# Performance work log

Hardware: AMD Instinct MI355X
Metric: run time of the kernel (lower is better)

Reference implementation:

```python
import jax, jax.numpy as jnp
import numpy as np

K = 20  # number of nearest neighbors (includes self, distance 0, as in torch topk(largest=False))


def edge_feature(x, k):
    """x: (B, C, N) -> edge features (B, N, k, 2C) = concat[central, neighbor - central]."""
    sq = jnp.sum(x * x, axis=1)                       # (B, N)
    inner = jnp.einsum('bcn,bcm->bnm', x, x)          # (B, N, N)
    d = sq[:, :, None] + sq[:, None, :] - 2.0 * inner # squared pairwise distance
    _, idx = jax.lax.top_k(-d, k)                     # (B, N, k) nearest indices (incl. self)
    xT = jnp.transpose(x, (0, 2, 1))                  # (B, N, C)
    # nb[b,n,j,c] = xT[b, idx[b,n,j], c]
    nb = jnp.take_along_axis(xT[:, :, None, :], idx[:, :, :, None], axis=1)  # (B, N, k, C)
    central = jnp.broadcast_to(xT[:, :, None, :], nb.shape)
    return jnp.concatenate([central, nb - central], axis=-1)  # (B, N, k, 2C)


def setup_inputs() -> dict:
    key = jax.random.key(0)
    ks = jax.random.split(key, 13)
    B, C, N = 8, 3, 4096
    def w(k_, shape, fan_in):
        return (jax.random.normal(k_, shape, dtype=jnp.float32) / np.sqrt(fan_in)).astype(jnp.float32)
    inp = {
        'x':  jax.random.normal(ks[0], (B, C, N), dtype=jnp.float32),
        # local 1x1 conv2d weights (out_ch, in_ch)
        'W1': w(ks[1], (64, 6), 6),        'b1': jnp.zeros((64,), jnp.float32),
        'W2': w(ks[2], (128, 64), 64),     'b2': jnp.zeros((128,), jnp.float32),
        # inter 1x1 conv1d
        'W3': w(ks[3], (1024, 128), 128),  'b3': jnp.zeros((1024,), jnp.float32),
        # global FC
        'W4': w(ks[4], (512, 1024), 1024), 'b4': jnp.zeros((512,), jnp.float32),
        'W5': w(ks[5], (256, 512), 512),   'b5': jnp.zeros((256,), jnp.float32),
        # final linear (torch inits this to zeros -> identity output; use small random for a
        # non-trivial correctness baseline, same math path)
        'W6': 0.01 * w(ks[6], (9, 256), 256), 'b6': jnp.zeros((9,), jnp.float32),
    }
    return inp


def reference(x, W1, b1, W2, b2, W3, b3, W4, b4, W5, b5, W6, b6):
    e = edge_feature(x, K)                                     # (B, N, k, 6)
    h = jax.nn.relu(jnp.einsum('bnkc,oc->bnko', e, W1) + b1)   # (B, N, k, 64)
    h = jax.nn.relu(jnp.einsum('bnkc,oc->bnko', h, W2) + b2)   # (B, N, k, 128)
    h = jnp.max(h, axis=2)                                     # max over k -> (B, N, 128)
    h = jax.nn.relu(jnp.einsum('bnc,oc->bno', h, W3) + b3)     # (B, N, 1024)
    g = jnp.max(h, axis=1)                                     # max over points -> (B, 1024)
    g = jax.nn.relu(g @ W4.T + b4)                             # (B, 512)
    g = jax.nn.relu(g @ W5.T + b5)                             # (B, 256)
    t = g @ W6.T + b6                                          # (B, 9)
    Bsz = x.shape[0]
    out_ch, in_ch = 3, 3
    t = t.reshape(Bsz, out_ch, in_ch) + jnp.eye(out_ch, in_ch, dtype=t.dtype)
    return t
```

## Files before the change

kernel.cpp:

```cpp
#include <hip/hip_runtime.h>
#include <hip/hip_bf16.h>
#include <cstdint>

#define B_SZ 8
#define NPTS 4096
#define KNN  20
#define NTOT (B_SZ * NPTS)
#define PPB  8

typedef unsigned int uint;
typedef unsigned short ushort;
using short8 = __attribute__((ext_vector_type(8))) short;
using f32x4  = __attribute__((ext_vector_type(4))) float;

__device__ __forceinline__ ushort f2bf(float f) {
  uint u = __float_as_uint(f);
  u += 0x7fff + ((u >> 16) & 1);
  return (ushort)(u >> 16);
}
__device__ __forceinline__ float bf2f(ushort h) {
  return __uint_as_float(((uint)h) << 16);
}
__device__ __forceinline__ uint fenc(float f) {
  uint u = __float_as_uint(f);
  return (u & 0x80000000u) ? ~u : (u | 0x80000000u);
}
__device__ __forceinline__ float fdec(uint e) {
  uint u = (e & 0x80000000u) ? (e & 0x7fffffffu) : ~e;
  return __uint_as_float(u);
}

__device__ __forceinline__ void sortf64(float& v, int lane) {
  #pragma unroll
  for (int k = 2; k <= 64; k <<= 1) {
    #pragma unroll
    for (int j = k >> 1; j > 0; j >>= 1) {
      float o = __shfl_xor(v, j, 64);
      bool keepmin = (((lane & k) == 0) == ((lane & j) == 0));
      bool lt = v < o;
      v = (keepmin == lt) ? v : o;
    }
  }
}

__device__ __forceinline__ void sortu64(unsigned long long& v, int lane) {
  #pragma unroll
  for (int k = 2; k <= 64; k <<= 1) {
    #pragma unroll
    for (int j = k >> 1; j > 0; j >>= 1) {
      unsigned long long o = __shfl_xor(v, j, 64);
      bool keepmin = (((lane & k) == 0) == ((lane & j) == 0));
      bool lt = v < o;
      v = (keepmin == lt) ? v : o;
    }
  }
}

__global__ __launch_bounds__(256, 4) void knn_prep_kernel(
    const float* __restrict__ x,  const float* __restrict__ W1,
    const float* __restrict__ W3, const float* __restrict__ W2,
    ushort* __restrict__ u, ushort* __restrict__ W3b, ushort* __restrict__ W2b,
    int* __restrict__ idx_out) {
  __shared__ int surv[4][256];
  __shared__ int cnt[4];

  if (blockIdx.x >= 8192) {
    int blk = blockIdx.x - 8192;
    if (blk < 1024) {
      int t = blk * 256 + threadIdx.x;
      int p = t >> 3, c0 = (t & 7) * 8;
      int b = p >> 12, n = p & (NPTS - 1);
      const float* xb = x + (size_t)b * 3 * NPTS;
      float x0 = xb[n], x1 = xb[NPTS + n], x2 = xb[2 * NPTS + n];
      uint pk[4];
      #pragma unroll
      for (int j = 0; j < 8; ++j) {
        const float* w = W1 + (c0 + j) * 6;
        float v = w[3] * x0 + w[4] * x1 + w[5] * x2;
        ushort h = f2bf(v);
        if (j & 1) pk[j >> 1] |= ((uint)h << 16); else pk[j >> 1] = h;
      }
      uint4 q; q.x = pk[0]; q.y = pk[1]; q.z = pk[2]; q.w = pk[3];
      *reinterpret_cast<uint4*>(u + (size_t)p * 64 + c0) = q;
    } else if (blk < 1088) {
      int t = (blk - 1024) * 256 + threadIdx.x;
      const float4* src = reinterpret_cast<const float4*>(W3 + t * 8);
      float4 f0 = src[0], f1 = src[1];
      uint4 pk;
      pk.x = (uint)f2bf(f0.x) | ((uint)f2bf(f0.y) << 16);
      pk.y = (uint)f2bf(f0.z) | ((uint)f2bf(f0.w) << 16);
      pk.z = (uint)f2bf(f1.x) | ((uint)f2bf(f1.y) << 16);
      pk.w = (uint)f2bf(f1.z) | ((uint)f2bf(f1.w) << 16);
      *reinterpret_cast<uint4*>(W3b + t * 8) = pk;
    } else {
      int t = (blk - 1088) * 256 + threadIdx.x;
      const float4* src = reinterpret_cast<const float4*>(W2 + t * 8);
      float4 f0 = src[0], f1 = src[1];
      uint4 pk;
      pk.x = (uint)f2bf(f0.x) | ((uint)f2bf(f0.y) << 16);
      pk.y = (uint)f2bf(f0.z) | ((uint)f2bf(f0.w) << 16);
      pk.z = (uint)f2bf(f1.x) | ((uint)f2bf(f1.y) << 16);
      pk.w = (uint)f2bf(f1.z) | ((uint)f2bf(f1.w) << 16);
      *reinterpret_cast<uint4*>(W2b + t * 8) = pk;
    }
    return;
  }

  const unsigned long long INFK = ~0ull;
  int w = threadIdx.x >> 6, lane = threadIdx.x & 63;
  int row = blockIdx.x * 4 + w;
  int b = row >> 12, n = row & (NPTS - 1);
  const float* xb = x + (size_t)b * 3 * NPTS;
  float qx = xb[n], qy = xb[NPTS + n], qz = xb[2 * NPTS + n];
  if (lane == 0) cnt[w] = 0;

  const float4* X0 = reinterpret_cast<const float4*>(xb);
  const float4* X1 = reinterpret_cast<const float4*>(xb + NPTS);
  const float4* X2 = reinterpret_cast<const float4*>(xb + 2 * NPTS);

  uint kreg[32];
  float bm = 3.0e38f;
  #pragma unroll
  for (int i = 0; i < 16; ++i) {
    int v4 = i * 64 + lane;
    float4 a0 = X0[v4], a1 = X1[v4], a2 = X2[v4];
    float dx, dy, dz, d0, d1, d2, d3;
    dx = a0.x - qx; dy = a1.x - qy; dz = a2.x - qz; d0 = dx*dx + dy*dy + dz*dz;
    dx = a0.y - qx; dy = a1.y - qy; dz = a2.y - qz; d1 = dx*dx + dy*dy + dz*dz;
    dx = a0.z - qx; dy = a1.z - qy; dz = a2.z - qz; d2 = dx*dx + dy*dy + dz*dz;
    dx = a0.w - qx; dy = a1.w - qy; dz = a2.w - qz; d3 = dx*dx + dy*dy + dz*dz;
    bm = fminf(bm, fminf(fminf(d0, d1), fminf(d2, d3)));
    kreg[2*i]   = (__float_as_uint(d0) >> 16) | (__float_as_uint(d1) & 0xFFFF0000u);
    kreg[2*i+1] = (__float_as_uint(d2) >> 16) | (__float_as_uint(d3) & 0xFFFF0000u);
  }

  sortf64(bm, lane);
  float T = __shfl(bm, 19, 64);
  uint T16 = __float_as_uint(T) >> 16;

  asm volatile("s_waitcnt lgkmcnt(0)" ::: "memory");
  #pragma unroll
  for (int i = 0; i < 16; ++i) {
    uint ka = kreg[2*i], kb = kreg[2*i+1];
    int m0 = (i * 64 + lane) * 4;
    if ((ka & 0xffffu) <= T16) { int s = atomicAdd(&cnt[w], 1); if (s < 256) surv[w][s] = m0; }
    if ((ka >> 16)     <= T16) { int s = atomicAdd(&cnt[w], 1); if (s < 256) surv[w][s] = m0 + 1; }
    if ((kb & 0xffffu) <= T16) { int s = atomicAdd(&cnt[w], 1); if (s < 256) surv[w][s] = m0 + 2; }
    if ((kb >> 16)     <= T16) { int s = atomicAdd(&cnt[w], 1); if (s < 256) surv[w][s] = m0 + 3; }
  }
  asm volatile("s_waitcnt lgkmcnt(0)" ::: "memory");
  int M = cnt[w];

  if (M <= 256) {
    unsigned long long run = INFK;
    int nch = (M + 63) >> 6;
    for (int c = 0; c < nch; ++c) {
      int s = c * 64 + lane;
      unsigned long long v = INFK;
      if (s < M) {
        int m = surv[w][s];
        float dx = xb[m] - qx, dy = xb[NPTS + m] - qy, dz = xb[2 * NPTS + m] - qz;
        float d = dx * dx + dy * dy + dz * dz;
        v = ((unsigned long long)__float_as_uint(d) << 32) | (unsigned)m;
      }
      sortu64(v, lane);
      if (c == 0) {
        run = v;
      } else {
        unsigned long long b19 = __shfl(v, (19 - lane) & 63, 64);
        unsigned long long cand = run < b19 ? run : b19;
        run = (lane < KNN) ? cand : INFK;
        sortu64(run, lane);
      }
    }
    if (lane < KNN) idx_out[(size_t)row * KNN + lane] = (int)(run & 0xFFFFFFFFull);
  } else {
    unsigned long long prev = 0ull;
    for (int r = 0; r < KNN; ++r) {
      unsigned long long best = INFK;
      for (int i = 0; i < 16; ++i) {
        int v4 = i * 64 + lane;
        float4 a0 = X0[v4], a1 = X1[v4], a2 = X2[v4];
        float dx, dy, dz, d[4];
        dx = a0.x - qx; dy = a1.x - qy; dz = a2.x - qz; d[0] = dx*dx + dy*dy + dz*dz;
        dx = a0.y - qx; dy = a1.y - qy; dz = a2.y - qz; d[1] = dx*dx + dy*dy + dz*dz;
        dx = a0.z - qx; dy = a1.z - qy; dz = a2.z - qz; d[2] = dx*dx + dy*dy + dz*dz;
        dx = a0.w - qx; dy = a1.w - qy; dz = a2.w - qz; d[3] = dx*dx + dy*dy + dz*dz;
        #pragma unroll
        for (int j = 0; j < 4; ++j) {
          int m = i * 256 + lane * 4 + j;
          unsigned long long key =
              ((unsigned long long)__float_as_uint(d[j]) << 32) | (unsigned)m;
          if ((r == 0 || key > prev) && key < best) best = key;
        }
      }
      #pragma unroll
      for (int off = 32; off; off >>= 1) {
        unsigned long long o = __shfl_xor(best, off, 64);
        best = o < best ? o : best;
      }
      if (lane == 0) idx_out[(size_t)row * KNN + r] = (int)(best & 0xFFFFFFFFull);
      prev = best;
    }
  }
}

__global__ __launch_bounds__(256, 4) void edge_kernel(
    const float* __restrict__ x,  const float* __restrict__ W1, const float* __restrict__ b1,
    const ushort* __restrict__ W2b, const float* __restrict__ b2,
    const ushort* __restrict__ u, const int* __restrict__ idx,
    float* __restrict__ h128) {
  __shared__ __align__(16) char h1s[PPB * 32 * 128];
  __shared__ float vs[PPB * 64];
  __shared__ int   nbs[PPB * KNN];

  int tid = threadIdx.x, w = tid >> 6, l = tid & 63;
  int p0 = blockIdx.x * PPB;
  int b = p0 >> 12;
  const float* xb = x + (size_t)b * 3 * NPTS;

  for (int t = tid; t < PPB * 64; t += 256) {
    int p = t >> 6, c = t & 63;
    int n = (p0 + p) & (NPTS - 1);
    float x0 = xb[n], x1 = xb[NPTS + n], x2 = xb[2 * NPTS + n];
    const float* wr = W1 + c * 6;
    vs[t] = (wr[0] - wr[3]) * x0 + (wr[1] - wr[4]) * x1 + (wr[2] - wr[5]) * x2 + b1[c];
  }
  if (tid < PPB * KNN) nbs[tid] = idx[(size_t)p0 * KNN + tid];

  short8 bfr[8][2];
  #pragma unroll
  for (int nt = 0; nt < 8; ++nt) {
    #pragma unroll
    for (int ks = 0; ks < 2; ++ks) {
      bfr[nt][ks] = *(const short8*)(W2b + (nt * 16 + (l & 15)) * 64
                                         + ks * 32 + (l >> 4) * 8);
    }
  }
  __syncthreads();

  const ushort* ub = u + (((size_t)b) << 12) * 64;
  #pragma unroll
  for (int j = 0; j < 8; ++j) {
    int e_loc = j * 8 + (l >> 3);
    int p_loc = (w << 1) + (e_loc >> 5);
    int e_in = e_loc & 31;
    int e_src = (e_in < KNN) ? e_in : e_in - KNN;
    int nb = nbs[p_loc * KNN + e_src];
    int c0 = (l & 7) * 8;
    uint4 uv = *(const uint4*)(ub + (((size_t)nb) << 6) + c0);
    const float* vp = vs + p_loc * 64 + c0;
    float4 v0 = *(const float4*)vp, v1 = *(const float4*)(vp + 4);
    float h0 = fmaxf(bf2f((ushort)(uv.x & 0xffff)) + v0.x, 0.f);
    float h1 = fmaxf(bf2f((ushort)(uv.x >> 16))    + v0.y, 0.f);
    float h2 = fmaxf(bf2f((ushort)(uv.y & 0xffff)) + v0.z, 0.f);
    float h3 = fmaxf(bf2f((ushort)(uv.y >> 16))    + v0.w, 0.f);
    float h4 = fmaxf(bf2f((ushort)(uv.z & 0xffff)) + v1.x, 0.f);
    float h5 = fmaxf(bf2f((ushort)(uv.z >> 16))    + v1.y, 0.f);
    float h6 = fmaxf(bf2f((ushort)(uv.w & 0xffff)) + v1.z, 0.f);
    float h7 = fmaxf(bf2f((ushort)(uv.w >> 16))    + v1.w, 0.f);
    uint4 pk;
    pk.x = (uint)f2bf(h0) | ((uint)f2bf(h1) << 16);
    pk.y = (uint)f2bf(h2) | ((uint)f2bf(h3) << 16);
    pk.z = (uint)f2bf(h4) | ((uint)f2bf(h5) << 16);
    pk.w = (uint)f2bf(h6) | ((uint)f2bf(h7) << 16);
    int row = (w << 6) + e_loc;
    int byte = (row * 128 + c0 * 2) ^ ((row & 7) << 4);
    *(uint4*)(h1s + byte) = pk;
  }
  __syncthreads();

  float bias0 = b2[l], bias1 = b2[64 + l];

  #pragma unroll
  for (int pt = 0; pt < 2; ++pt) {
    int rbase = (w << 6) + (pt << 5);
    short8 a[2][2];
    #pragma unroll
    for (int m = 0; m < 2; ++m) {
      #pragma unroll
      for (int ks = 0; ks < 2; ++ks) {
        int row = rbase + m * 16 + (l & 15);
        int byte = (row * 128 + ks * 64 + (l >> 4) * 16) ^ ((row & 7) << 4);
        a[m][ks] = *(const short8*)(h1s + byte);
      }
    }
    float r03 = 0.f, r47 = 0.f;
    #pragma unroll
    for (int nt = 0; nt < 8; ++nt) {
      f32x4 acc0 = {0.f, 0.f, 0.f, 0.f}, acc1 = {0.f, 0.f, 0.f, 0.f};
      acc0 = __builtin_amdgcn_mfma_f32_16x16x32_bf16(a[0][0], bfr[nt][0], acc0, 0, 0, 0);
      acc0 = __builtin_amdgcn_mfma_f32_16x16x32_bf16(a[0][1], bfr[nt][1], acc0, 0, 0, 0);
      acc1 = __builtin_amdgcn_mfma_f32_16x16x32_bf16(a[1][0], bfr[nt][0], acc1, 0, 0, 0);
      acc1 = __builtin_amdgcn_mfma_f32_16x16x32_bf16(a[1][1], bfr[nt][1], acc1, 0, 0, 0);
      float m0 = fmaxf(fmaxf(fmaxf(acc0[0], acc1[0]), fmaxf(acc0[1], acc1[1])),
                       fmaxf(fmaxf(acc0[2], acc1[2]), fmaxf(acc0[3], acc1[3])));
      m0 = fmaxf(m0, __shfl_xor(m0, 16, 64));
      m0 = fmaxf(m0, __shfl_xor(m0, 32, 64));
      if ((l >> 4) == (nt & 3)) { if (nt < 4) r03 = m0; else r47 = m0; }
    }
    int pg = p0 + (w << 1) + pt;
    h128[(size_t)pg * 128 + l]      = fmaxf(r03 + bias0, 0.f);
    h128[(size_t)pg * 128 + 64 + l] = fmaxf(r47 + bias1, 0.f);
  }
}

__global__ __launch_bounds__(256, 2) void inter_kernel(
    const float* __restrict__ h128, const ushort* __restrict__ W3b,
    uint* __restrict__ g_enc) {
  __shared__ __align__(16) char as_[32 * 256];
  int tid = threadIdx.x, w = tid >> 6, l = tid & 63;
  int chunk = blockIdx.x;
  const float* hp = h128 + (size_t)chunk * 32 * 128;

  {
    int row = tid >> 3, c0 = (tid & 7) * 16;
    const float4* src = reinterpret_cast<const float4*>(hp + row * 128 + c0);
    float4 f0 = src[0], f1 = src[1], f2 = src[2], f3 = src[3];
    uint4 p0, p1;
    p0.x = (uint)f2bf(f0.x) | ((uint)f2bf(f0.y) << 16);
    p0.y = (uint)f2bf(f0.z) | ((uint)f2bf(f0.w) << 16);
    p0.z = (uint)f2bf(f1.x) | ((uint)f2bf(f1.y) << 16);
    p0.w = (uint)f2bf(f1.z) | ((uint)f2bf(f1.w) << 16);
    p1.x = (uint)f2bf(f2.x) | ((uint)f2bf(f2.y) << 16);
    p1.y = (uint)f2bf(f2.z) | ((uint)f2bf(f2.w) << 16);
    p1.z = (uint)f2bf(f3.x) | ((uint)f2bf(f3.y) << 16);
    p1.w = (uint)f2bf(f3.z) | ((uint)f2bf(f3.w) << 16);
    int sw = (row & 7) << 4;
    *(uint4*)(as_ + ((row * 256 + c0 * 2) ^ sw))      = p0;
    *(uint4*)(as_ + ((row * 256 + c0 * 2 + 16) ^ sw)) = p1;
  }
  __syncthreads();

  short8 a[2][4];
  #pragma unroll
  for (int m = 0; m < 2; ++m) {
    #pragma unroll
    for (int ks = 0; ks < 4; ++ks) {
      int row = m * 16 + (l & 15);
      int byte = (row * 256 + ks * 64 + (l >> 4) * 16) ^ ((row & 7) << 4);
      a[m][ks] = *(const short8*)(as_ + byte);
    }
  }

  const ushort* wb = W3b + (size_t)(w * 256) * 128;
  float res[4];
  #pragma unroll
  for (int nt = 0; nt < 16; ++nt) {
    f32x4 acc0 = {0.f, 0.f, 0.f, 0.f}, acc1 = {0.f, 0.f, 0.f, 0.f};
    #pragma unroll
    for (int ks = 0; ks < 4; ++ks) {
      short8 bf = *(const short8*)(wb + (size_t)(nt * 16 + (l & 15)) * 128
                                      + ks * 32 + (l >> 4) * 8);
      acc0 = __builtin_amdgcn_mfma_f32_16x16x32_bf16(a[0][ks], bf, acc0, 0, 0, 0);
      acc1 = __builtin_amdgcn_mfma_f32_16x16x32_bf16(a[1][ks], bf, acc1, 0, 0, 0);
    }
    float m0 = fmaxf(fmaxf(fmaxf(acc0[0], acc1[0]), fmaxf(acc0[1], acc1[1])),
                     fmaxf(fmaxf(acc0[2], acc1[2]), fmaxf(acc0[3], acc1[3])));
    m0 = fmaxf(m0, __shfl_xor(m0, 16, 64));
    m0 = fmaxf(m0, __shfl_xor(m0, 32, 64));
    if ((l >> 4) == (nt & 3)) res[nt >> 2] = m0;
  }
  uint* ge = g_enc + (size_t)(chunk >> 7) * 1024 + w * 256;
  #pragma unroll
  for (int g = 0; g < 4; ++g) atomicMax(ge + g * 64 + l, fenc(res[g]));
}

__global__ __launch_bounds__(64) void fc_kernel(const float* __restrict__ in,
                                                const uint* __restrict__ enc,
                                                const float* __restrict__ pre_b,
                                                const float* __restrict__ W,
                                                const float* __restrict__ bias,
                                                float* __restrict__ out,
                                                int in_dim, int out_dim, int mode) {
  int blk = blockIdx.x;
  int b = blk / out_dim, o = blk % out_dim;
  int lane = threadIdx.x;
  const float* w = W + (size_t)o * in_dim;
  float s = 0.f;
  for (int c = lane; c < in_dim; c += 64) {
    float v;
    if (mode == 2) v = fmaxf(fdec(enc[(size_t)b * in_dim + c]) + pre_b[c], 0.f);
    else           v = in[(size_t)b * in_dim + c];
    s += v * w[c];
  }
  #pragma unroll
  for (int off = 32; off; off >>= 1) s += __shfl_down(s, off);
  if (lane == 0) {
    float r = s + bias[o];
    if (mode != 1) r = fmaxf(r, 0.0f);
    else if (o == 0 || o == 4 || o == 8) r += 1.0f;
    out[blk] = r;
  }
}

extern "C" void kernel_launch(void* const* d_in, const int* in_sizes, int n_in,
                              void* d_out, int out_size, void* d_ws, size_t ws_size,
                              hipStream_t stream) {
  const float* x  = (const float*)d_in[0];
  const float* W1 = (const float*)d_in[1];
  const float* b1 = (const float*)d_in[2];
  const float* W2 = (const float*)d_in[3];
  const float* b2 = (const float*)d_in[4];
  const float* W3 = (const float*)d_in[5];
  const float* b3 = (const float*)d_in[6];
  const float* W4 = (const float*)d_in[7];
  const float* b4 = (const float*)d_in[8];
  const float* W5 = (const float*)d_in[9];
  const float* b5 = (const float*)d_in[10];
  const float* W6 = (const float*)d_in[11];
  const float* b6 = (const float*)d_in[12];
  float* out = (float*)d_out;

  char* ws = (char*)d_ws;
  ushort* u_bf = (ushort*)(ws);
  int*   idxb  = (int*)  (ws + (8u  << 20));
  float* h128  = (float*)(ws + (11u << 20));
  ushort* W3b  = (ushort*)(ws + (27u << 20));
  ushort* W2b  = (ushort*)(ws + (27u << 20) + (256u << 10));
  uint*  g_enc = (uint*) (ws + (5u  << 20));
  float* g4    = (float*)(ws + (6u  << 20));
  float* g5    = (float*)(ws + (7u  << 20));

  hipMemsetAsync(g_enc, 0, B_SZ * 1024 * sizeof(uint), stream);
  hipLaunchKernelGGL(knn_prep_kernel, dim3(8192 + 1092), dim3(256), 0, stream,
                     x, W1, W3, W2, u_bf, W3b, W2b, idxb);
  hipLaunchKernelGGL(edge_kernel, dim3(NTOT / PPB), dim3(256), 0, stream,
                     x, W1, b1, W2b, b2, u_bf, idxb, h128);
  hipLaunchKernelGGL(inter_kernel, dim3(1024), dim3(256), 0, stream, h128, W3b, g_enc);
  hipLaunchKernelGGL(fc_kernel, dim3(B_SZ * 512), dim3(64), 0, stream,
                     nullptr, g_enc, b3, W4, b4, g4, 1024, 512, 2);
  hipLaunchKernelGGL(fc_kernel, dim3(B_SZ * 256), dim3(64), 0, stream,
                     g4, nullptr, nullptr, W5, b5, g5, 512, 256, 0);
  hipLaunchKernelGGL(fc_kernel, dim3(B_SZ * 9),   dim3(64), 0, stream,
                     g5, nullptr, nullptr, W6, b6, out, 256, 9, 1);
}
```

Measured before the change: 189.7 us.

## Store edge output as bf16, double inter tile rows, fold memset into prep

The edge kernel now writes its 128-channel max-pooled features as bf16, not fp32. This halves that intermediate's write and read traffic and removes the conversion step in inter_kernel. inter_kernel processes 64 points per block with four MFMA accumulators, halving the grid and the atomicMax count, at the cost of more registers and shared memory. The g_enc zeroing moves from a separate memset into an extra prep block placed at the front of the knn_prep grid, which risks little since later kernels run after it.

```diff
diff --git a/kernel.cpp b/kernel.cpp
--- a/kernel.cpp
+++ b/kernel.cpp
@@ -7,6 +7,7 @@
 #define KNN  20
 #define NTOT (B_SZ * NPTS)
 #define PPB  8
+#define NPREP 1093
 
 typedef unsigned int uint;
 typedef unsigned short ushort;
@@ -60,12 +61,12 @@
     const float* __restrict__ x,  const float* __restrict__ W1,
     const float* __restrict__ W3, const float* __restrict__ W2,
     ushort* __restrict__ u, ushort* __restrict__ W3b, ushort* __restrict__ W2b,
-    int* __restrict__ idx_out) {
+    uint* __restrict__ g_enc, int* __restrict__ idx_out) {
   __shared__ int surv[4][256];
   __shared__ int cnt[4];
 
-  if (blockIdx.x >= 8192) {
-    int blk = blockIdx.x - 8192;
+  if (blockIdx.x < NPREP) {
+    int blk = blockIdx.x;
     if (blk < 1024) {
       int t = blk * 256 + threadIdx.x;
       int p = t >> 3, c0 = (t & 7) * 8;
@@ -92,7 +93,7 @@
       pk.z = (uint)f2bf(f1.x) | ((uint)f2bf(f1.y) << 16);
       pk.w = (uint)f2bf(f1.z) | ((uint)f2bf(f1.w) << 16);
       *reinterpret_cast<uint4*>(W3b + t * 8) = pk;
-    } else {
+    } else if (blk < 1092) {
       int t = (blk - 1088) * 256 + threadIdx.x;
       const float4* src = reinterpret_cast<const float4*>(W2 + t * 8);
       float4 f0 = src[0], f1 = src[1];
@@ -102,13 +103,15 @@
       pk.z = (uint)f2bf(f1.x) | ((uint)f2bf(f1.y) << 16);
       pk.w = (uint)f2bf(f1.z) | ((uint)f2bf(f1.w) << 16);
       *reinterpret_cast<uint4*>(W2b + t * 8) = pk;
+    } else {
+      for (int i = threadIdx.x; i < B_SZ * 1024; i += 256) g_enc[i] = 0;
     }
     return;
   }
 
   const unsigned long long INFK = ~0ull;
   int w = threadIdx.x >> 6, lane = threadIdx.x & 63;
-  int row = blockIdx.x * 4 + w;
+  int row = (blockIdx.x - NPREP) * 4 + w;
   int b = row >> 12, n = row & (NPTS - 1);
   const float* xb = x + (size_t)b * 3 * NPTS;
   float qx = xb[n], qy = xb[NPTS + n], qz = xb[2 * NPTS + n];
@@ -209,7 +212,7 @@
     const float* __restrict__ x,  const float* __restrict__ W1, const float* __restrict__ b1,
     const ushort* __restrict__ W2b, const float* __restrict__ b2,
     const ushort* __restrict__ u, const int* __restrict__ idx,
-    float* __restrict__ h128) {
+    ushort* __restrict__ h128b) {
   __shared__ __align__(16) char h1s[PPB * 32 * 128];
   __shared__ float vs[PPB * 64];
   __shared__ int   nbs[PPB * KNN];
@@ -300,41 +303,33 @@
       if ((l >> 4) == (nt & 3)) { if (nt < 4) r03 = m0; else r47 = m0; }
     }
     int pg = p0 + (w << 1) + pt;
-    h128[(size_t)pg * 128 + l]      = fmaxf(r03 + bias0, 0.f);
-    h128[(size_t)pg * 128 + 64 + l] = fmaxf(r47 + bias1, 0.f);
+    h128b[(size_t)pg * 128 + l]      = f2bf(fmaxf(r03 + bias0, 0.f));
+    h128b[(size_t)pg * 128 + 64 + l] = f2bf(fmaxf(r47 + bias1, 0.f));
   }
 }
 
 __global__ __launch_bounds__(256, 2) void inter_kernel(
-    const float* __restrict__ h128, const ushort* __restrict__ W3b,
+    const ushort* __restrict__ h128b, const ushort* __restrict__ W3b,
     uint* __restrict__ g_enc) {
-  __shared__ __align__(16) char as_[32 * 256];
+  __shared__ __align__(16) char as_[64 * 256];
   int tid = threadIdx.x, w = tid >> 6, l = tid & 63;
   int chunk = blockIdx.x;
-  const float* hp = h128 + (size_t)chunk * 32 * 128;
+  const ushort* hp = h128b + (size_t)chunk * 64 * 128;
 
   {
-    int row = tid >> 3, c0 = (tid & 7) * 16;
-    const float4* src = reinterpret_cast<const float4*>(hp + row * 128 + c0);
-    float4 f0 = src[0], f1 = src[1], f2 = src[2], f3 = src[3];
-    uint4 p0, p1;
-    p0.x = (uint)f2bf(f0.x) | ((uint)f2bf(f0.y) << 16);
-    p0.y = (uint)f2bf(f0.z) | ((uint)f2bf(f0.w) << 16);
-    p0.z = (uint)f2bf(f1.x) | ((uint)f2bf(f1.y) << 16);
-    p0.w = (uint)f2bf(f1.z) | ((uint)f2bf(f1.w) << 16);
-    p1.x = (uint)f2bf(f2.x) | ((uint)f2bf(f2.y) << 16);
-    p1.y = (uint)f2bf(f2.z) | ((uint)f2bf(f2.w) << 16);
-    p1.z = (uint)f2bf(f3.x) | ((uint)f2bf(f3.y) << 16);
-    p1.w = (uint)f2bf(f3.z) | ((uint)f2bf(f3.w) << 16);
+    int row = tid >> 2, q = tid & 3;
+    const uint4* src = reinterpret_cast<const uint4*>(hp + row * 128 + q * 32);
     int sw = (row & 7) << 4;
-    *(uint4*)(as_ + ((row * 256 + c0 * 2) ^ sw))      = p0;
-    *(uint4*)(as_ + ((row * 256 + c0 * 2 + 16) ^ sw)) = p1;
+    int base = row * 256 + q * 64;
+    #pragma unroll
+    for (int k = 0; k < 4; ++k)
+      *(uint4*)(as_ + ((base + k * 16) ^ sw)) = src[k];
   }
   __syncthreads();
 
-  short8 a[2][4];
-  #pragma unroll
-  for (int m = 0; m < 2; ++m) {
+  short8 a[4][4];
+  #pragma unroll
+  for (int m = 0; m < 4; ++m) {
     #pragma unroll
     for (int ks = 0; ks < 4; ++ks) {
       int row = m * 16 + (l & 15);
@@ -347,21 +342,27 @@
   float res[4];
   #pragma unroll
   for (int nt = 0; nt < 16; ++nt) {
-    f32x4 acc0 = {0.f, 0.f, 0.f, 0.f}, acc1 = {0.f, 0.f, 0.f, 0.f};
+    f32x4 acc0 = {0.f,0.f,0.f,0.f}, acc1 = {0.f,0.f,0.f,0.f};
+    f32x4 acc2 = {0.f,0.f,0.f,0.f}, acc3 = {0.f,0.f,0.f,0.f};
     #pragma unroll
     for (int ks = 0; ks < 4; ++ks) {
       short8 bf = *(const short8*)(wb + (size_t)(nt * 16 + (l & 15)) * 128
                                       + ks * 32 + (l >> 4) * 8);
       acc0 = __builtin_amdgcn_mfma_f32_16x16x32_bf16(a[0][ks], bf, acc0, 0, 0, 0);
       acc1 = __builtin_amdgcn_mfma_f32_16x16x32_bf16(a[1][ks], bf, acc1, 0, 0, 0);
-    }
-    float m0 = fmaxf(fmaxf(fmaxf(acc0[0], acc1[0]), fmaxf(acc0[1], acc1[1])),
-                     fmaxf(fmaxf(acc0[2], acc1[2]), fmaxf(acc0[3], acc1[3])));
+      acc2 = __builtin_amdgcn_mfma_f32_16x16x32_bf16(a[2][ks], bf, acc2, 0, 0, 0);
+      acc3 = __builtin_amdgcn_mfma_f32_16x16x32_bf16(a[3][ks], bf, acc3, 0, 0, 0);
+    }
+    float m01 = fmaxf(fmaxf(fmaxf(acc0[0], acc1[0]), fmaxf(acc0[1], acc1[1])),
+                      fmaxf(fmaxf(acc0[2], acc1[2]), fmaxf(acc0[3], acc1[3])));
+    float m23 = fmaxf(fmaxf(fmaxf(acc2[0], acc3[0]), fmaxf(acc2[1], acc3[1])),
+                      fmaxf(fmaxf(acc2[2], acc3[2]), fmaxf(acc2[3], acc3[3])));
+    float m0 = fmaxf(m01, m23);
     m0 = fmaxf(m0, __shfl_xor(m0, 16, 64));
     m0 = fmaxf(m0, __shfl_xor(m0, 32, 64));
     if ((l >> 4) == (nt & 3)) res[nt >> 2] = m0;
   }
-  uint* ge = g_enc + (size_t)(chunk >> 7) * 1024 + w * 256;
+  uint* ge = g_enc + (size_t)(chunk >> 6) * 1024 + w * 256;
   #pragma unroll
   for (int g = 0; g < 4; ++g) atomicMax(ge + g * 64 + l, fenc(res[g]));
 }
@@ -413,21 +414,20 @@
   float* out = (float*)d_out;
 
   char* ws = (char*)d_ws;
-  ushort* u_bf = (ushort*)(ws);
-  int*   idxb  = (int*)  (ws + (8u  << 20));
-  float* h128  = (float*)(ws + (11u << 20));
-  ushort* W3b  = (ushort*)(ws + (27u << 20));
-  ushort* W2b  = (ushort*)(ws + (27u << 20) + (256u << 10));
-  uint*  g_enc = (uint*) (ws + (5u  << 20));
-  float* g4    = (float*)(ws + (6u  << 20));
-  float* g5    = (float*)(ws + (7u  << 20));
-
-  hipMemsetAsync(g_enc, 0, B_SZ * 1024 * sizeof(uint), stream);
-  hipLaunchKernelGGL(knn_prep_kernel, dim3(8192 + 1092), dim3(256), 0, stream,
-                     x, W1, W3, W2, u_bf, W3b, W2b, idxb);
+  ushort* u_bf  = (ushort*)(ws);
+  int*    idxb  = (int*)  (ws + (8u  << 20));
+  ushort* h128b = (ushort*)(ws + (11u << 20));
+  ushort* W3b   = (ushort*)(ws + (27u << 20));
+  ushort* W2b   = (ushort*)(ws + (27u << 20) + (256u << 10));
+  uint*   g_enc = (uint*) (ws + (5u  << 20));
+  float*  g4    = (float*)(ws + (6u  << 20));
+  float*  g5    = (float*)(ws + (7u  << 20));
+
+  hipLaunchKernelGGL(knn_prep_kernel, dim3(NPREP + 8192), dim3(256), 0, stream,
+                     x, W1, W3, W2, u_bf, W3b, W2b, g_enc, idxb);
   hipLaunchKernelGGL(edge_kernel, dim3(NTOT / PPB), dim3(256), 0, stream,
-                     x, W1, b1, W2b, b2, u_bf, idxb, h128);
-  hipLaunchKernelGGL(inter_kernel, dim3(1024), dim3(256), 0, stream, h128, W3b, g_enc);
+                     x, W1, b1, W2b, b2, u_bf, idxb, h128b);
+  hipLaunchKernelGGL(inter_kernel, dim3(512), dim3(256), 0, stream, h128b, W3b, g_enc);
   hipLaunchKernelGGL(fc_kernel, dim3(B_SZ * 512), dim3(64), 0, stream,
                      nullptr, g_enc, b3, W4, b4, g4, 1024, 512, 2);
   hipLaunchKernelGGL(fc_kernel, dim3(B_SZ * 256), dim3(64), 0, stream,
```

Result: faster. 168.7 us (-11.0%).
